# Kernel optimization log

Measured on AMD Instinct MI355X. Metric: run time of the kernel, lower is better.

## Reference

```python
import jax, jax.numpy as jnp
import numpy as np

B, N, C, K = 2, 4096, 256, 64


def setup_inputs() -> dict:
    key = jax.random.key(0)
    k1, k2, k3, k4, k5, k6 = jax.random.split(key, 6)
    points = jax.random.normal(k1, (B, N, 3), dtype=jnp.float32)  # ~N(0,1) cloud
    point_features = jax.random.normal(k2, (B, N, C), dtype=jnp.float32)
    # proposals: centers inside the cloud, positive box dims, random yaw (unused by mask math)
    centers = jax.random.uniform(k3, (B, K, 3), minval=-1.0, maxval=1.0, dtype=jnp.float32)
    dims = jax.random.uniform(k4, (B, K, 3), minval=0.5, maxval=1.5, dtype=jnp.float32)
    ry = jax.random.uniform(k5, (B, K, 1), minval=-np.pi, maxval=np.pi, dtype=jnp.float32)
    proposals = jnp.concatenate([centers, dims, ry], axis=-1)  # (B,K,7)
    W1 = jax.random.normal(k6, (C, 256), dtype=jnp.float32) * (1.0 / np.sqrt(C))
    b1 = jnp.zeros((256,), dtype=jnp.float32)
    W2 = jax.random.normal(jax.random.fold_in(key, 7), (256, 256), dtype=jnp.float32) * (1.0 / 16.0)
    b2 = jnp.zeros((256,), dtype=jnp.float32)
    return {"points": points, "point_features": point_features, "proposals": proposals,
            "W1": W1, "b1": b1, "W2": W2, "b2": b2}


def reference(points, point_features, proposals, W1, b1, W2, b2):
    # points: (B,N,3), point_features: (B,N,C), proposals: (B,K,7)
    ctr = proposals[..., :3]                      # (B,K,3) cx,cy,cz
    half = proposals[..., 3:6] * 0.5              # (B,K,3) l/2,w/2,h/2
    lo = ctr - half                               # (B,K,3)
    hi = ctr + half
    # point-in-box mask (axis-aligned, strict inequalities as in source): (B,K,N)
    p = points[:, None, :, :]                     # (B,1,N,3)
    mask = jnp.all((p > lo[:, :, None, :]) & (p < hi[:, :, None, :]), axis=-1)
    any_in = jnp.any(mask, axis=-1)               # (B,K)
    # masked max-pool over points: (B,K,N,C) -> (B,K,C)
    neg_inf = jnp.asarray(-jnp.inf, point_features.dtype)
    masked = jnp.where(mask[..., None], point_features[:, None, :, :], neg_inf)
    pooled = jnp.max(masked, axis=2)
    pooled = jnp.where(any_in[..., None], pooled, 0.0)  # empty box -> zeros
    # fc: Linear(C,256) + ReLU + Linear(256,256) + ReLU
    h = jax.nn.relu(jnp.einsum('bkc,cd->bkd', pooled, W1) + b1)
    out = jax.nn.relu(jnp.einsum('bkd,de->bke', h, W2) + b2)
    return out
```

## Files before the change

### kernel.cpp

```cpp
#include <hip/hip_runtime.h>

#define Bn 2
#define Nn 4096
#define Cn 256
#define Kn 64
#define BK (Bn * Kn)
#define NW 16
#define BT 1024
#define PAD (7 * NW)

__device__ __forceinline__ float4 max4(float4 a, float4 b) {
    return make_float4(fmaxf(a.x, b.x), fmaxf(a.y, b.y),
                       fmaxf(a.z, b.z), fmaxf(a.w, b.w));
}

__global__ __launch_bounds__(BT) void fused_roi_kernel(
    const float* __restrict__ points,
    const float* __restrict__ feats,
    const float* __restrict__ proposals,
    const float* __restrict__ W1,
    const float* __restrict__ b1,
    const float* __restrict__ W2,
    const float* __restrict__ b2,
    float* __restrict__ out)
{
    const int bk   = blockIdx.x;
    const int b    = bk / Kn;
    const int tid  = threadIdx.x;
    const int w    = tid >> 6;
    const int lane = tid & 63;

    __shared__ int   s_idx[Nn + PAD];
    __shared__ int   s_count;
    __shared__ float s_part[NW][Cn];
    __shared__ float s_vec[Cn];
    __shared__ float s_red[4][Cn];

    const float* prop = proposals + (size_t)bk * 7;
    const float cx = prop[0], cy = prop[1], cz = prop[2];
    const float hx = prop[3] * 0.5f, hy = prop[4] * 0.5f, hz = prop[5] * 0.5f;
    const float lox = cx - hx, loy = cy - hy, loz = cz - hz;
    const float hix = cx + hx, hiy = cy + hy, hiz = cz + hz;

    if (tid == 0) s_count = 0;
    __syncthreads();

    {
        const float4* pv = (const float4*)(points + (size_t)b * Nn * 3);
        const float4 q0 = pv[3 * tid + 0];
        const float4 q1 = pv[3 * tid + 1];
        const float4 q2 = pv[3 * tid + 2];
        const int n0 = 4 * tid;

        const bool in0 = (q0.x > lox) & (q0.x < hix) &
                         (q0.y > loy) & (q0.y < hiy) &
                         (q0.z > loz) & (q0.z < hiz);
        const bool in1 = (q0.w > lox) & (q0.w < hix) &
                         (q1.x > loy) & (q1.x < hiy) &
                         (q1.y > loz) & (q1.y < hiz);
        const bool in2 = (q1.z > lox) & (q1.z < hix) &
                         (q1.w > loy) & (q1.w < hiy) &
                         (q2.x > loz) & (q2.x < hiz);
        const bool in3 = (q2.y > lox) & (q2.y < hix) &
                         (q2.z > loy) & (q2.z < hiy) &
                         (q2.w > loz) & (q2.w < hiz);

        if (in0) s_idx[atomicAdd(&s_count, 1)] = n0 + 0;
        if (in1) s_idx[atomicAdd(&s_count, 1)] = n0 + 1;
        if (in2) s_idx[atomicAdd(&s_count, 1)] = n0 + 2;
        if (in3) s_idx[atomicAdd(&s_count, 1)] = n0 + 3;
    }
    __syncthreads();
    const int count = s_count;

    if (count > 0 && tid < PAD) s_idx[count + tid] = s_idx[0];
    __syncthreads();

    const float* fb = feats + (size_t)b * Nn * Cn;
    float4 mx = make_float4(-INFINITY, -INFINITY, -INFINITY, -INFINITY);
    for (int i = w; i < count; i += 8 * NW) {
        const int a0 = s_idx[i + 0 * NW], a1 = s_idx[i + 1 * NW];
        const int a2 = s_idx[i + 2 * NW], a3 = s_idx[i + 3 * NW];
        const int a4 = s_idx[i + 4 * NW], a5 = s_idx[i + 5 * NW];
        const int a6 = s_idx[i + 6 * NW], a7 = s_idx[i + 7 * NW];
        const float4 f0 = *(const float4*)(fb + (size_t)a0 * Cn + lane * 4);
        const float4 f1 = *(const float4*)(fb + (size_t)a1 * Cn + lane * 4);
        const float4 f2 = *(const float4*)(fb + (size_t)a2 * Cn + lane * 4);
        const float4 f3 = *(const float4*)(fb + (size_t)a3 * Cn + lane * 4);
        const float4 f4 = *(const float4*)(fb + (size_t)a4 * Cn + lane * 4);
        const float4 f5 = *(const float4*)(fb + (size_t)a5 * Cn + lane * 4);
        const float4 f6 = *(const float4*)(fb + (size_t)a6 * Cn + lane * 4);
        const float4 f7 = *(const float4*)(fb + (size_t)a7 * Cn + lane * 4);
        mx = max4(mx, max4(max4(f0, f1), max4(f2, f3)));
        mx = max4(mx, max4(max4(f4, f5), max4(f6, f7)));
    }
    *(float4*)&s_part[w][lane * 4] = mx;
    __syncthreads();

    if (tid < Cn) {
        float m = s_part[0][tid];
        #pragma unroll
        for (int k = 1; k < NW; ++k) m = fmaxf(m, s_part[k][tid]);
        if (m == -INFINITY) m = 0.0f;
        s_vec[tid] = m;
    }
    __syncthreads();

    {
        const int g = tid >> 8;
        const int d = tid & 255;
        const float* w1 = W1 + (size_t)(g * 64) * 256 + d;
        const float* sv = s_vec + g * 64;
        float acc = 0.0f;
        #pragma unroll 16
        for (int c = 0; c < 64; ++c) {
            acc = fmaf(sv[c], w1[(size_t)c * 256], acc);
        }
        s_red[g][d] = acc;
    }
    __syncthreads();
    if (tid < Cn) {
        const float h = fmaxf(
            b1[tid] + ((s_red[0][tid] + s_red[1][tid]) +
                       (s_red[2][tid] + s_red[3][tid])), 0.0f);
        s_vec[tid] = h;
    }
    __syncthreads();

    {
        const int g = tid >> 8;
        const int d = tid & 255;
        const float* w2 = W2 + (size_t)(g * 64) * 256 + d;
        const float* sv = s_vec + g * 64;
        float acc = 0.0f;
        #pragma unroll 16
        for (int c = 0; c < 64; ++c) {
            acc = fmaf(sv[c], w2[(size_t)c * 256], acc);
        }
        s_red[g][d] = acc;
    }
    __syncthreads();
    if (tid < Cn) {
        out[(size_t)bk * 256 + tid] = fmaxf(
            b2[tid] + ((s_red[0][tid] + s_red[1][tid]) +
                       (s_red[2][tid] + s_red[3][tid])), 0.0f);
    }
}

extern "C" void kernel_launch(void* const* d_in, const int* in_sizes, int n_in,
                              void* d_out, int out_size, void* d_ws, size_t ws_size,
                              hipStream_t stream) {
    const float* points    = (const float*)d_in[0];
    const float* feats     = (const float*)d_in[1];
    const float* proposals = (const float*)d_in[2];
    const float* W1        = (const float*)d_in[3];
    const float* b1        = (const float*)d_in[4];
    const float* W2        = (const float*)d_in[5];
    const float* b2        = (const float*)d_in[6];
    float* out             = (float*)d_out;
    (void)d_ws; (void)ws_size;

    fused_roi_kernel<<<BK, BT, 0, stream>>>(points, feats, proposals,
                                            W1, b1, W2, b2, out);
}
```

Before: 80.72 us.

## Split pooling across two blocks per box and use wave-ballot compaction

The fused kernel becomes two kernels. The first launches two blocks per proposal, each scanning half the points and max-pooling features into a partial buffer in workspace. The second combines the two partials and runs the two-layer MLP. Index compaction now uses wave ballots and popcounts with one atomic per wave instead of one per point. The aim is more parallelism with only 128 blocks on a many-CU GPU and less atomic contention, at the cost of an extra launch and a partial round-trip through global memory. Only half the threads do the scan in each pooling block.

After: 82.58 us. +2.3%, slower.

```diff
diff --git a/kernel.cpp b/kernel.cpp
--- a/kernel.cpp
+++ b/kernel.cpp
@@ -7,6 +7,7 @@
 #define BK (Bn * Kn)
 #define NW 16
 #define BT 1024
+#define HALF (Nn / 2)
 #define PAD (7 * NW)
 
 __device__ __forceinline__ float4 max4(float4 a, float4 b) {
@@ -14,27 +15,23 @@
                        fmaxf(a.z, b.z), fmaxf(a.w, b.w));
 }
 
-__global__ __launch_bounds__(BT) void fused_roi_kernel(
+__global__ __launch_bounds__(BT) void pool_half_kernel(
     const float* __restrict__ points,
     const float* __restrict__ feats,
     const float* __restrict__ proposals,
-    const float* __restrict__ W1,
-    const float* __restrict__ b1,
-    const float* __restrict__ W2,
-    const float* __restrict__ b2,
-    float* __restrict__ out)
+    float* __restrict__ partial)
 {
-    const int bk   = blockIdx.x;
+    const int blk  = blockIdx.x;
+    const int bk   = blk >> 1;
+    const int half = blk & 1;
     const int b    = bk / Kn;
     const int tid  = threadIdx.x;
     const int w    = tid >> 6;
     const int lane = tid & 63;
 
-    __shared__ int   s_idx[Nn + PAD];
+    __shared__ int   s_idx[HALF + PAD];
     __shared__ int   s_count;
     __shared__ float s_part[NW][Cn];
-    __shared__ float s_vec[Cn];
-    __shared__ float s_red[4][Cn];
 
     const float* prop = proposals + (size_t)bk * 7;
     const float cx = prop[0], cy = prop[1], cz = prop[2];
@@ -45,12 +42,13 @@
     if (tid == 0) s_count = 0;
     __syncthreads();
 
-    {
-        const float4* pv = (const float4*)(points + (size_t)b * Nn * 3);
+    if (tid < 512) {
+        const int n0 = half * HALF + 4 * tid;
+        const float4* pv = (const float4*)(points + (size_t)b * Nn * 3
+                                           + (size_t)half * HALF * 3);
         const float4 q0 = pv[3 * tid + 0];
         const float4 q1 = pv[3 * tid + 1];
         const float4 q2 = pv[3 * tid + 2];
-        const int n0 = 4 * tid;
 
         const bool in0 = (q0.x > lox) & (q0.x < hix) &
                          (q0.y > loy) & (q0.y < hiy) &
@@ -65,10 +63,24 @@
                          (q2.z > loy) & (q2.z < hiy) &
                          (q2.w > loz) & (q2.w < hiz);
 
-        if (in0) s_idx[atomicAdd(&s_count, 1)] = n0 + 0;
-        if (in1) s_idx[atomicAdd(&s_count, 1)] = n0 + 1;
-        if (in2) s_idx[atomicAdd(&s_count, 1)] = n0 + 2;
-        if (in3) s_idx[atomicAdd(&s_count, 1)] = n0 + 3;
+        const unsigned long long m0 = __ballot(in0);
+        const unsigned long long m1 = __ballot(in1);
+        const unsigned long long m2 = __ballot(in2);
+        const unsigned long long m3 = __ballot(in3);
+        const int c0 = __popcll(m0), c1 = __popcll(m1);
+        const int c2 = __popcll(m2), c3 = __popcll(m3);
+
+        int base = 0;
+        if (lane == 0) base = atomicAdd(&s_count, c0 + c1 + c2 + c3);
+        base = __shfl(base, 0);
+
+        const unsigned long long below = (lane == 63)
+            ? 0xFFFFFFFFFFFFFFFFull >> 1
+            : ((1ull << lane) - 1);
+        if (in0) s_idx[base + __popcll(m0 & below)] = n0 + 0;
+        if (in1) s_idx[base + c0 + __popcll(m1 & below)] = n0 + 1;
+        if (in2) s_idx[base + c0 + c1 + __popcll(m2 & below)] = n0 + 2;
+        if (in3) s_idx[base + c0 + c1 + c2 + __popcll(m3 & below)] = n0 + 3;
     }
     __syncthreads();
     const int count = s_count;
@@ -101,42 +113,58 @@
         float m = s_part[0][tid];
         #pragma unroll
         for (int k = 1; k < NW; ++k) m = fmaxf(m, s_part[k][tid]);
+        partial[(size_t)blk * Cn + tid] = m;
+    }
+}
+
+__global__ __launch_bounds__(BT) void reduce_mlp_kernel(
+    const float* __restrict__ partial,
+    const float* __restrict__ W1,
+    const float* __restrict__ b1,
+    const float* __restrict__ W2,
+    const float* __restrict__ b2,
+    float* __restrict__ out)
+{
+    const int bk  = blockIdx.x;
+    const int tid = threadIdx.x;
+    const int g   = tid >> 8;
+    const int d   = tid & 255;
+
+    __shared__ float s_vec[Cn];
+    __shared__ float s_red[4][Cn];
+
+    if (tid < Cn) {
+        float m = fmaxf(partial[(size_t)(2 * bk) * Cn + tid],
+                        partial[(size_t)(2 * bk + 1) * Cn + tid]);
         if (m == -INFINITY) m = 0.0f;
         s_vec[tid] = m;
     }
     __syncthreads();
 
     {
-        const int g = tid >> 8;
-        const int d = tid & 255;
         const float* w1 = W1 + (size_t)(g * 64) * 256 + d;
         const float* sv = s_vec + g * 64;
         float acc = 0.0f;
         #pragma unroll 16
-        for (int c = 0; c < 64; ++c) {
+        for (int c = 0; c < 64; ++c)
             acc = fmaf(sv[c], w1[(size_t)c * 256], acc);
-        }
         s_red[g][d] = acc;
     }
     __syncthreads();
     if (tid < Cn) {
-        const float h = fmaxf(
+        s_vec[tid] = fmaxf(
             b1[tid] + ((s_red[0][tid] + s_red[1][tid]) +
                        (s_red[2][tid] + s_red[3][tid])), 0.0f);
-        s_vec[tid] = h;
     }
     __syncthreads();
 
     {
-        const int g = tid >> 8;
-        const int d = tid & 255;
         const float* w2 = W2 + (size_t)(g * 64) * 256 + d;
         const float* sv = s_vec + g * 64;
         float acc = 0.0f;
         #pragma unroll 16
-        for (int c = 0; c < 64; ++c) {
+        for (int c = 0; c < 64; ++c)
             acc = fmaf(sv[c], w2[(size_t)c * 256], acc);
-        }
         s_red[g][d] = acc;
     }
     __syncthreads();
@@ -158,8 +186,9 @@
     const float* W2        = (const float*)d_in[5];
     const float* b2        = (const float*)d_in[6];
     float* out             = (float*)d_out;
-    (void)d_ws; (void)ws_size;
+    float* partial         = (float*)d_ws;
 
-    fused_roi_kernel<<<BK, BT, 0, stream>>>(points, feats, proposals,
-                                            W1, b1, W2, b2, out);
+    pool_half_kernel<<<2 * BK, BT, 0, stream>>>(points, feats, proposals,
+                                                partial);
+    reduce_mlp_kernel<<<BK, BT, 0, stream>>>(partial, W1, b1, W2, b2, out);
 }
```
